# Kernel tuning notes

Hardware: AMD Instinct MI355X
Metric: run time of the kernel (lower is better)

The kernel has to match this reference:

```python
import jax, jax.numpy as jnp
import numpy as np

B, S, HID = 2, 2048, 2048
NH, NKV, HD = 16, 2, 128
N_REP = NH // NKV
SCALE = HD ** -0.5
NEG = -1e9


def rotate_half(x):
    x1, x2 = x[..., : HD // 2], x[..., HD // 2 :]
    return jnp.concatenate((-x2, x1), axis=-1)


def setup_inputs() -> dict:
    key = jax.random.key(0)
    ks = jax.random.split(key, 8)
    hidden_states = jax.random.normal(ks[0], (B, S, HID), jnp.float32)
    # RoPE tables (theta=10000), shape [B, S, HD]
    inv_freq = 1.0 / (10000.0 ** (np.arange(0, HD, 2, dtype=np.float32) / HD))
    pos = np.arange(S, dtype=np.float32)
    freqs = np.outer(pos, inv_freq)  # [S, HD/2]
    emb = np.concatenate([freqs, freqs], axis=-1)  # [S, HD]
    cos = jnp.broadcast_to(jnp.asarray(np.cos(emb)), (B, S, HD))
    sin = jnp.broadcast_to(jnp.asarray(np.sin(emb)), (B, S, HD))
    # additive causal mask [B, 1, S, S]
    causal = jnp.where(jnp.tril(jnp.ones((S, S), bool)), 0.0, NEG).astype(jnp.float32)
    attention_mask = jnp.broadcast_to(causal[None, None], (B, 1, S, S))
    sc = 0.02
    return {
        "hidden_states": hidden_states,
        "cos": cos,
        "sin": sin,
        "attention_mask": attention_mask,
        "Wq": jax.random.normal(ks[1], (NH * HD, HID), jnp.float32) * sc,
        "bq": jax.random.normal(ks[2], (NH * HD,), jnp.float32) * sc,
        "Wk": jax.random.normal(ks[3], (NKV * HD, HID), jnp.float32) * sc,
        "bk": jax.random.normal(ks[4], (NKV * HD,), jnp.float32) * sc,
        "Wv": jax.random.normal(ks[5], (NKV * HD, HID), jnp.float32) * sc,
        "bv": jax.random.normal(ks[6], (NKV * HD,), jnp.float32) * sc,
        "Wo": jax.random.normal(ks[7], (HID, NH * HD), jnp.float32) * sc,
    }


def reference(hidden_states, cos, sin, attention_mask, Wq, bq, Wk, bk, Wv, bv, Wo):
    b, s, _ = hidden_states.shape
    # QKV projections -> [B, H, S, D]
    q = (hidden_states @ Wq.T + bq).reshape(b, s, NH, HD).transpose(0, 2, 1, 3)
    k = (hidden_states @ Wk.T + bk).reshape(b, s, NKV, HD).transpose(0, 2, 1, 3)
    v = (hidden_states @ Wv.T + bv).reshape(b, s, NKV, HD).transpose(0, 2, 1, 3)
    # RoPE (cos/sin unsqueezed at head dim)
    c, si = cos[:, None], sin[:, None]
    q = q * c + rotate_half(q) * si
    k = k * c + rotate_half(k) * si
    # GQA: repeat kv heads
    k = jnp.repeat(k, N_REP, axis=1)
    v = jnp.repeat(v, N_REP, axis=1)
    scores = jnp.einsum("bhqd,bhkd->bhqk", q, k) * SCALE
    scores = scores + attention_mask[:, :, :, :s]
    attn_weights = jax.nn.softmax(scores.astype(jnp.float32), axis=-1).astype(q.dtype)
    attn_out = jnp.einsum("bhqk,bhkd->bhqd", attn_weights, v)
    attn_out = attn_out.transpose(0, 2, 1, 3).reshape(b, s, NH * HD)
    out = attn_out @ Wo.T
    return out, attn_weights
```

## Files before the change

kernel.cpp:

```cpp
#include <hip/hip_runtime.h>
#include <hip/hip_bf16.h>
#include <cstdint>

constexpr int Bb  = 2;
constexpr int Ss  = 2048;
constexpr int HID = 2048;
constexpr int NH  = 16;
constexpr int NKV = 2;
constexpr int HD  = 128;
constexpr int Mrows = Bb * Ss;
constexpr float SCALE = 0.08838834764831845f;

typedef __bf16 bf16_t;
typedef __attribute__((ext_vector_type(8))) __bf16 bf16x8;
typedef __attribute__((ext_vector_type(4))) __bf16 bf16x4;
typedef __attribute__((ext_vector_type(4))) float f32x4;

static __device__ __forceinline__ f32x4 mfma16(bf16x8 a, bf16x8 b, f32x4 c) {
  return __builtin_amdgcn_mfma_f32_16x16x32_bf16(a, b, c, 0, 0, 0);
}

static __device__ __forceinline__ void stage_async(bf16_t* lds, const bf16_t* src,
                                                   int ld, int tid) {
#pragma unroll
  for (int it = 0; it < 2; ++it) {
    int c = tid + it * 256;
    int row = c >> 2, kc = c & 3;
    __builtin_amdgcn_global_load_lds(
        (const __attribute__((address_space(1))) void*)(src + (size_t)row * ld + kc * 8),
        (__attribute__((address_space(3))) void*)(lds + c * 8), 16, 0, 0);
  }
}

template <int IM, int JM>
static __device__ __forceinline__ void wave_mma(const bf16_t* As, const bf16_t* Bs,
                                                f32x4 (&acc)[IM][JM], int wm, int wn,
                                                int lane) {
  const int q = lane >> 4, r = lane & 15;
  bf16x8 a[IM], b[JM];
#pragma unroll
  for (int i = 0; i < IM; ++i)
    a[i] = *(const bf16x8*)(As + (wm + i * 16 + r) * 32 + q * 8);
#pragma unroll
  for (int j = 0; j < JM; ++j)
    b[j] = *(const bf16x8*)(Bs + (wn + j * 16 + r) * 32 + q * 8);
#pragma unroll
  for (int i = 0; i < IM; ++i)
#pragma unroll
    for (int j = 0; j < JM; ++j)
      acc[i][j] = mfma16(a[i], b[j], acc[i][j]);
}

__global__ void cvt_bf16_kernel(const float* __restrict__ in, bf16_t* __restrict__ out) {
  size_t i = ((size_t)blockIdx.x * 256 + threadIdx.x) * 8;
  float4 a = *(const float4*)(in + i);
  float4 b = *(const float4*)(in + i + 4);
  bf16x8 v;
  v[0] = (__bf16)a.x; v[1] = (__bf16)a.y; v[2] = (__bf16)a.z; v[3] = (__bf16)a.w;
  v[4] = (__bf16)b.x; v[5] = (__bf16)b.y; v[6] = (__bf16)b.z; v[7] = (__bf16)b.w;
  *(bf16x8*)(out + i) = v;
}

__global__ void zero_kernel(float* __restrict__ p) {
  p[(size_t)blockIdx.x * 256 + threadIdx.x] = 0.0f;
}

__global__ __launch_bounds__(256) void proj_kernel(
    const bf16_t* __restrict__ A, const bf16_t* __restrict__ Bt,
    const float* __restrict__ bq, const float* __restrict__ bk,
    const float* __restrict__ bv, const float* __restrict__ cosb,
    const float* __restrict__ sinb, bf16_t* __restrict__ q_bf,
    bf16_t* __restrict__ k_bf, bf16_t* __restrict__ v_t) {
  __shared__ __align__(16) bf16_t As[128 * 32];
  __shared__ __align__(16) bf16_t Bs[128 * 32];
  const int tid = threadIdx.x;
  const int bx = blockIdx.x;
  const int m0 = blockIdx.y * 128, n0 = bx * 128;
  const int lane = tid & 63, w = tid >> 6;
  const int wm = w * 32;
  const int q = lane >> 4, r = lane & 15;
  f32x4 acc[2][8];
#pragma unroll
  for (int i = 0; i < 2; ++i)
#pragma unroll
    for (int j = 0; j < 8; ++j) acc[i][j] = (f32x4){0.f, 0.f, 0.f, 0.f};
  const bf16_t* Ap = A + (size_t)m0 * HID;
  const bf16_t* Bp = Bt + (size_t)n0 * HID;
  for (int k0 = 0; k0 < HID; k0 += 32) {
    stage_async(As, Ap + k0, HID, tid);
    stage_async(Bs, Bp + k0, HID, tid);
    __syncthreads();
    wave_mma<2, 8>(As, Bs, acc, wm, 0, lane);
    __syncthreads();
  }
  const float* bias_base;
  int mode;
  int hh;
  if (bx < 16) { mode = 0; hh = bx; bias_base = bq + n0; }
  else if (bx < 18) { mode = 1; hh = bx - 16; bias_base = bk + (bx - 16) * 128; }
  else { mode = 2; hh = bx - 18; bias_base = bv + (bx - 18) * 128; }
  float bias_j[8];
#pragma unroll
  for (int j = 0; j < 8; ++j) bias_j[j] = bias_base[j * 16 + r];
  float e[2][8][4];
#pragma unroll
  for (int i = 0; i < 2; ++i)
#pragma unroll
    for (int j = 0; j < 8; ++j)
#pragma unroll
      for (int t = 0; t < 4; ++t) e[i][j][t] = acc[i][j][t] + bias_j[j];

  if (mode == 2) {
#pragma unroll
    for (int i = 0; i < 2; ++i) {
      int s_base = m0 + wm + i * 16 + q * 4;
      int bI = s_base >> 11, s = s_base & 2047;
#pragma unroll
      for (int j = 0; j < 8; ++j) {
        int d = j * 16 + r;
        bf16x4 pk;
#pragma unroll
        for (int t = 0; t < 4; ++t) pk[t] = (__bf16)e[i][j][t];
        *(bf16x4*)(v_t + ((size_t)(bI * NKV + hh) * HD + d) * Ss + s) = pk;
      }
    }
  } else {
    bf16_t* dst_base = (mode == 0) ? q_bf : k_bf;
    const int nhv = (mode == 0) ? NH : NKV;
#pragma unroll
    for (int i = 0; i < 2; ++i) {
#pragma unroll
      for (int t = 0; t < 4; ++t) {
        int s_glob = m0 + wm + i * 16 + q * 4 + t;
        int bI = s_glob >> 11, s = s_glob & 2047;
        const float* cp = cosb + ((size_t)bI * Ss + s) * HD;
        const float* sp = sinb + ((size_t)bI * Ss + s) * HD;
        bf16_t* dst = dst_base + ((size_t)(bI * nhv + hh) * Ss + s) * HD;
#pragma unroll
        for (int j = 0; j < 8; ++j) {
          int d = j * 16 + r;
          float c = cp[d], sn = sp[d];
          float p = e[i][j ^ 4][t];
          float o = e[i][j][t] * c + ((j < 4) ? -p : p) * sn;
          dst[d] = (__bf16)o;
        }
      }
    }
  }
}

__global__ __launch_bounds__(256) void qk_kernel(const bf16_t* __restrict__ qb,
                                                 const bf16_t* __restrict__ kb,
                                                 float* __restrict__ attn,
                                                 float* __restrict__ rowsum) {
  const int tj = blockIdx.x, ti = blockIdx.y;
  if (tj > ti) return;
  const int bh = blockIdx.z;
  const int b = bh >> 4, h = bh & 15, kv = h >> 3;
  __shared__ __align__(16) bf16_t As[128 * 32];
  __shared__ __align__(16) bf16_t Bs[128 * 32];
  __shared__ float rs[128];
  const int tid = threadIdx.x;
  if (tid < 128) rs[tid] = 0.0f;
  const int lane = tid & 63, w = tid >> 6;
  const int wm = (w >> 1) * 64, wn = (w & 1) * 64;
  const int q = lane >> 4, r = lane & 15;
  f32x4 acc[4][4];
#pragma unroll
  for (int i = 0; i < 4; ++i)
#pragma unroll
    for (int j = 0; j < 4; ++j) acc[i][j] = (f32x4){0.f, 0.f, 0.f, 0.f};
  const bf16_t* Ap = qb + (size_t)bh * Ss * HD + (size_t)ti * 128 * HD;
  const bf16_t* Bp = kb + (size_t)(b * NKV + kv) * Ss * HD + (size_t)tj * 128 * HD;
#pragma unroll
  for (int k0 = 0; k0 < HD; k0 += 32) {
    stage_async(As, Ap + k0, HD, tid);
    stage_async(Bs, Bp + k0, HD, tid);
    __syncthreads();
    wave_mma<4, 4>(As, Bs, acc, wm, wn, lane);
    __syncthreads();
  }
  const bool diag = (ti == tj);
  float rp[4][4];
#pragma unroll
  for (int i = 0; i < 4; ++i)
#pragma unroll
    for (int t = 0; t < 4; ++t) rp[i][t] = 0.0f;
  float* orow = attn + ((size_t)bh * Ss + (size_t)ti * 128) * Ss + (size_t)tj * 128;
#pragma unroll
  for (int i = 0; i < 4; ++i) {
#pragma unroll
    for (int t = 0; t < 4; ++t) {
      int row_l = wm + i * 16 + q * 4 + t;
#pragma unroll
      for (int j = 0; j < 4; ++j) {
        int col_l = wn + j * 16 + r;
        float ev = (diag && col_l > row_l) ? 0.0f : __expf(acc[i][j][t] * SCALE);
        orow[(size_t)row_l * Ss + col_l] = ev;
        rp[i][t] += ev;
      }
    }
  }
#pragma unroll
  for (int off = 1; off < 16; off <<= 1)
#pragma unroll
    for (int i = 0; i < 4; ++i)
#pragma unroll
      for (int t = 0; t < 4; ++t) rp[i][t] += __shfl_xor(rp[i][t], off, 64);
  if (r == 0) {
#pragma unroll
    for (int i = 0; i < 4; ++i)
#pragma unroll
      for (int t = 0; t < 4; ++t)
        atomicAdd(&rs[wm + i * 16 + q * 4 + t], rp[i][t]);
  }
  __syncthreads();
  if (tid < 128)
    atomicAdd(rowsum + (size_t)bh * Ss + (size_t)ti * 128 + tid, rs[tid]);
}

__global__ __launch_bounds__(256) void pv_kernel(float* __restrict__ attn,
                                                 const bf16_t* __restrict__ vt,
                                                 const float* __restrict__ rowsum,
                                                 bf16_t* __restrict__ ao) {
  const int mt = blockIdx.y;
  const int bh = blockIdx.z;
  const int b = bh >> 4, h = bh & 15, kv = h >> 3;
  __shared__ __align__(16) bf16_t As[128 * 32];
  __shared__ __align__(16) bf16_t Bs[128 * 32];
  __shared__ float inv_s[128];
  const int tid = threadIdx.x;
  if (tid < 128)
    inv_s[tid] = 1.0f / rowsum[(size_t)bh * Ss + (size_t)mt * 128 + tid];
  __syncthreads();
  const int lane = tid & 63, w = tid >> 6;
  const int wm = (w >> 1) * 64, wn = (w & 1) * 64;
  const int q = lane >> 4, r = lane & 15;
  f32x4 acc[4][4];
#pragma unroll
  for (int i = 0; i < 4; ++i)
#pragma unroll
    for (int j = 0; j < 4; ++j) acc[i][j] = (f32x4){0.f, 0.f, 0.f, 0.f};
  float* Ap = attn + (size_t)bh * Ss * Ss + (size_t)mt * 128 * Ss;
  const bf16_t* Bp = vt + (size_t)(b * NKV + kv) * HD * Ss;
  const int kmax = (mt + 1) * 128;
  for (int k0 = 0; k0 < kmax; k0 += 32) {
#pragma unroll
    for (int it = 0; it < 2; ++it) {
      int c = tid + it * 256;
      int row = c >> 2, kc = c & 3;
      float* p = Ap + (size_t)row * Ss + k0 + kc * 8;
      float4 a = *(const float4*)p;
      float4 bq4 = *(const float4*)(p + 4);
      float inv = inv_s[row];
      a.x *= inv; a.y *= inv; a.z *= inv; a.w *= inv;
      bq4.x *= inv; bq4.y *= inv; bq4.z *= inv; bq4.w *= inv;
      *(float4*)p = a;
      *(float4*)(p + 4) = bq4;
      bf16x8 v8;
      v8[0] = (__bf16)a.x; v8[1] = (__bf16)a.y; v8[2] = (__bf16)a.z; v8[3] = (__bf16)a.w;
      v8[4] = (__bf16)bq4.x; v8[5] = (__bf16)bq4.y; v8[6] = (__bf16)bq4.z; v8[7] = (__bf16)bq4.w;
      *(bf16x8*)(As + c * 8) = v8;
    }
    stage_async(Bs, Bp + k0, Ss, tid);
    __syncthreads();
    wave_mma<4, 4>(As, Bs, acc, wm, wn, lane);
    __syncthreads();
  }
  const int width = Ss - kmax;
  if (width > 0) {
    const float4 z4 = {0.f, 0.f, 0.f, 0.f};
    for (int rr = 0; rr < 128; ++rr) {
      float* zp = Ap + (size_t)rr * Ss + kmax;
      for (int cc = tid * 4; cc < width; cc += 1024) *(float4*)(zp + cc) = z4;
    }
  }
#pragma unroll
  for (int i = 0; i < 4; ++i) {
#pragma unroll
    for (int t = 0; t < 4; ++t) {
      int row = mt * 128 + wm + i * 16 + q * 4 + t;
#pragma unroll
      for (int j = 0; j < 4; ++j) {
        int col = wn + j * 16 + r;
        ao[(((size_t)b * Ss + row) * NH + h) * HD + col] = (__bf16)acc[i][j][t];
      }
    }
  }
}

__global__ __launch_bounds__(256) void out_kernel(const bf16_t* __restrict__ A,
                                                  const bf16_t* __restrict__ Bt,
                                                  float* __restrict__ outp) {
  __shared__ __align__(16) bf16_t As[128 * 32];
  __shared__ __align__(16) bf16_t Bs[128 * 32];
  const int tid = threadIdx.x;
  const int m0 = blockIdx.y * 128, n0 = blockIdx.x * 128;
  const int lane = tid & 63, w = tid >> 6;
  const int wm = (w >> 1) * 64, wn = (w & 1) * 64;
  const int q = lane >> 4, r = lane & 15;
  f32x4 acc[4][4];
#pragma unroll
  for (int i = 0; i < 4; ++i)
#pragma unroll
    for (int j = 0; j < 4; ++j) acc[i][j] = (f32x4){0.f, 0.f, 0.f, 0.f};
  const bf16_t* Ap = A + (size_t)m0 * HID;
  const bf16_t* Bp = Bt + (size_t)n0 * HID;
  for (int k0 = 0; k0 < HID; k0 += 32) {
    stage_async(As, Ap + k0, HID, tid);
    stage_async(Bs, Bp + k0, HID, tid);
    __syncthreads();
    wave_mma<4, 4>(As, Bs, acc, wm, wn, lane);
    __syncthreads();
  }
#pragma unroll
  for (int i = 0; i < 4; ++i) {
#pragma unroll
    for (int t = 0; t < 4; ++t) {
      int row = m0 + wm + i * 16 + q * 4 + t;
#pragma unroll
      for (int j = 0; j < 4; ++j) {
        int col = n0 + wn + j * 16 + r;
        outp[(size_t)row * HID + col] = acc[i][j][t];
      }
    }
  }
}

extern "C" void kernel_launch(void* const* d_in, const int* in_sizes, int n_in,
                              void* d_out, int out_size, void* d_ws, size_t ws_size,
                              hipStream_t stream) {
  const float* hs   = (const float*)d_in[0];
  const float* cosb = (const float*)d_in[1];
  const float* sinb = (const float*)d_in[2];
  const float* Wq = (const float*)d_in[4];
  const float* bq = (const float*)d_in[5];
  const float* Wk = (const float*)d_in[6];
  const float* bk = (const float*)d_in[7];
  const float* Wv = (const float*)d_in[8];
  const float* bv = (const float*)d_in[9];
  const float* Wo = (const float*)d_in[10];

  float* out  = (float*)d_out;
  float* attn = out + (size_t)Bb * Ss * HID;

  char* wsp = (char*)d_ws;
  auto alloc = [&](size_t bytes) -> char* {
    char* p = wsp;
    wsp += (bytes + 255) & ~(size_t)255;
    return p;
  };
  bf16_t* hs_bf = (bf16_t*)alloc((size_t)Mrows * HID * 2);
  bf16_t* wqkv  = (bf16_t*)alloc((size_t)2560 * HID * 2);
  bf16_t* wo_bf = (bf16_t*)alloc((size_t)HID * NH * HD * 2);
  bf16_t* q_bf  = (bf16_t*)alloc((size_t)Mrows * NH * HD * 2);
  bf16_t* k_bf  = (bf16_t*)alloc((size_t)Bb * NKV * Ss * HD * 2);
  bf16_t* v_t   = (bf16_t*)alloc((size_t)Bb * NKV * Ss * HD * 2);
  bf16_t* ao_bf = (bf16_t*)alloc((size_t)Mrows * NH * HD * 2);
  float*  rs_ws = (float*)alloc((size_t)Bb * NH * Ss * 4);

  zero_kernel<<<(Bb * NH * Ss) / 256, 256, 0, stream>>>(rs_ws);

  cvt_bf16_kernel<<<(Mrows * HID) / 2048, 256, 0, stream>>>(hs, hs_bf);
  cvt_bf16_kernel<<<(NH * HD * HID) / 2048, 256, 0, stream>>>(Wq, wqkv);
  cvt_bf16_kernel<<<(NKV * HD * HID) / 2048, 256, 0, stream>>>(Wk, wqkv + (size_t)2048 * HID);
  cvt_bf16_kernel<<<(NKV * HD * HID) / 2048, 256, 0, stream>>>(Wv, wqkv + (size_t)2304 * HID);
  cvt_bf16_kernel<<<(HID * NH * HD) / 2048, 256, 0, stream>>>(Wo, wo_bf);

  proj_kernel<<<dim3(20, 32), 256, 0, stream>>>(hs_bf, wqkv, bq, bk, bv, cosb, sinb,
                                                q_bf, k_bf, v_t);

  qk_kernel<<<dim3(16, 16, Bb * NH), 256, 0, stream>>>(q_bf, k_bf, attn, rs_ws);

  pv_kernel<<<dim3(1, 16, Bb * NH), 256, 0, stream>>>(attn, v_t, rs_ws, ao_bf);

  out_kernel<<<dim3(16, 32), 256, 0, stream>>>(ao_bf, wo_bf, out);

  (void)in_sizes; (void)n_in; (void)out_size; (void)ws_size;
}
```

Baseline: 1.079 ms.

## Recompute QK scores in PV kernel instead of round-tripping fp32 attn matrix

The first pass now computes only the exp row sums and no longer writes the unnormalised scores. A new fused kernel recomputes QK^T per key tile, normalises with the precomputed row sums, writes the final attention weights once, and feeds them through LDS in bf16 straight into the PV matmul. This removes one full write plus a read and rewrite of the large fp32 attention matrix, at the cost of doing the QK matmul twice. The fused kernel also uses more LDS and registers, and its launch grid has only one block per query tile per head.

```diff
diff --git a/kernel.cpp b/kernel.cpp
--- a/kernel.cpp
+++ b/kernel.cpp
@@ -149,9 +149,8 @@
   }
 }
 
-__global__ __launch_bounds__(256) void qk_kernel(const bf16_t* __restrict__ qb,
+__global__ __launch_bounds__(256) void qs_kernel(const bf16_t* __restrict__ qb,
                                                  const bf16_t* __restrict__ kb,
-                                                 float* __restrict__ attn,
                                                  float* __restrict__ rowsum) {
   const int tj = blockIdx.x, ti = blockIdx.y;
   if (tj > ti) return;
@@ -186,7 +185,6 @@
   for (int i = 0; i < 4; ++i)
 #pragma unroll
     for (int t = 0; t < 4; ++t) rp[i][t] = 0.0f;
-  float* orow = attn + ((size_t)bh * Ss + (size_t)ti * 128) * Ss + (size_t)tj * 128;
 #pragma unroll
   for (int i = 0; i < 4; ++i) {
 #pragma unroll
@@ -196,7 +194,6 @@
       for (int j = 0; j < 4; ++j) {
         int col_l = wn + j * 16 + r;
         float ev = (diag && col_l > row_l) ? 0.0f : __expf(acc[i][j][t] * SCALE);
-        orow[(size_t)row_l * Ss + col_l] = ev;
         rp[i][t] += ev;
       }
     }
@@ -219,59 +216,121 @@
     atomicAdd(rowsum + (size_t)bh * Ss + (size_t)ti * 128 + tid, rs[tid]);
 }
 
-__global__ __launch_bounds__(256) void pv_kernel(float* __restrict__ attn,
-                                                 const bf16_t* __restrict__ vt,
-                                                 const float* __restrict__ rowsum,
-                                                 bf16_t* __restrict__ ao) {
+__global__ __launch_bounds__(256, 2) void spv_kernel(
+    const bf16_t* __restrict__ qb, const bf16_t* __restrict__ kb,
+    const bf16_t* __restrict__ vt, const float* __restrict__ rowsum,
+    float* __restrict__ attn, bf16_t* __restrict__ ao) {
   const int mt = blockIdx.y;
   const int bh = blockIdx.z;
   const int b = bh >> 4, h = bh & 15, kv = h >> 3;
-  __shared__ __align__(16) bf16_t As[128 * 32];
-  __shared__ __align__(16) bf16_t Bs[128 * 32];
+  __shared__ __align__(16) bf16_t Ks[4][128 * 32];
+  __shared__ __align__(16) bf16_t Ps[128 * 136];
   __shared__ float inv_s[128];
   const int tid = threadIdx.x;
   if (tid < 128)
     inv_s[tid] = 1.0f / rowsum[(size_t)bh * Ss + (size_t)mt * 128 + tid];
-  __syncthreads();
   const int lane = tid & 63, w = tid >> 6;
   const int wm = (w >> 1) * 64, wn = (w & 1) * 64;
   const int q = lane >> 4, r = lane & 15;
-  f32x4 acc[4][4];
+
+  const bf16_t* Qp = qb + (size_t)bh * Ss * HD + (size_t)mt * 128 * HD;
+#pragma unroll
+  for (int s = 0; s < 4; ++s) stage_async(Ks[s], Qp + s * 32, HD, tid);
+  __syncthreads();
+  bf16x8 aq[4][4];
+#pragma unroll
+  for (int s = 0; s < 4; ++s)
+#pragma unroll
+    for (int i = 0; i < 4; ++i)
+      aq[s][i] = *(const bf16x8*)(Ks[s] + (wm + i * 16 + r) * 32 + q * 8);
+  float inv_my[4][4];
 #pragma unroll
   for (int i = 0; i < 4; ++i)
 #pragma unroll
-    for (int j = 0; j < 4; ++j) acc[i][j] = (f32x4){0.f, 0.f, 0.f, 0.f};
-  float* Ap = attn + (size_t)bh * Ss * Ss + (size_t)mt * 128 * Ss;
-  const bf16_t* Bp = vt + (size_t)(b * NKV + kv) * HD * Ss;
+    for (int t = 0; t < 4; ++t)
+      inv_my[i][t] = inv_s[wm + i * 16 + q * 4 + t];
+  __syncthreads();
+
+  const bf16_t* Kp = kb + (size_t)(b * NKV + kv) * Ss * HD;
+  const bf16_t* Vp = vt + (size_t)(b * NKV + kv) * HD * Ss;
+  float* Arow = attn + ((size_t)bh * Ss + (size_t)mt * 128) * Ss;
+
+  f32x4 acc2[4][4];
+#pragma unroll
+  for (int i = 0; i < 4; ++i)
+#pragma unroll
+    for (int j = 0; j < 4; ++j) acc2[i][j] = (f32x4){0.f, 0.f, 0.f, 0.f};
+
+  for (int kt = 0; kt <= mt; ++kt) {
+#pragma unroll
+    for (int s = 0; s < 4; ++s)
+      stage_async(Ks[s], Kp + (size_t)kt * 128 * HD + s * 32, HD, tid);
+    __syncthreads();
+    f32x4 acc[4][4];
+#pragma unroll
+    for (int i = 0; i < 4; ++i)
+#pragma unroll
+      for (int j = 0; j < 4; ++j) acc[i][j] = (f32x4){0.f, 0.f, 0.f, 0.f};
+#pragma unroll
+    for (int s = 0; s < 4; ++s) {
+      bf16x8 bfr[4];
+#pragma unroll
+      for (int j = 0; j < 4; ++j)
+        bfr[j] = *(const bf16x8*)(Ks[s] + (wn + j * 16 + r) * 32 + q * 8);
+#pragma unroll
+      for (int i = 0; i < 4; ++i)
+#pragma unroll
+        for (int j = 0; j < 4; ++j)
+          acc[i][j] = mfma16(aq[s][i], bfr[j], acc[i][j]);
+    }
+    const bool diag = (kt == mt);
+#pragma unroll
+    for (int i = 0; i < 4; ++i) {
+#pragma unroll
+      for (int t = 0; t < 4; ++t) {
+        int row_l = wm + i * 16 + q * 4 + t;
+        float inv = inv_my[i][t];
+        float* orow = Arow + (size_t)row_l * Ss + kt * 128;
+#pragma unroll
+        for (int j = 0; j < 4; ++j) {
+          int col_l = wn + j * 16 + r;
+          float ev = (diag && col_l > row_l)
+                         ? 0.0f
+                         : __expf(acc[i][j][t] * SCALE) * inv;
+          orow[col_l] = ev;
+          Ps[row_l * 136 + col_l] = (__bf16)ev;
+        }
+      }
+    }
+    __syncthreads();
+#pragma unroll
+    for (int s = 0; s < 4; ++s)
+      stage_async(Ks[s], Vp + kt * 128 + s * 32, Ss, tid);
+    __syncthreads();
+#pragma unroll
+    for (int s = 0; s < 4; ++s) {
+      bf16x8 ap[4], bv4[4];
+#pragma unroll
+      for (int i = 0; i < 4; ++i)
+        ap[i] = *(const bf16x8*)(Ps + (wm + i * 16 + r) * 136 + s * 32 + q * 8);
+#pragma unroll
+      for (int j = 0; j < 4; ++j)
+        bv4[j] = *(const bf16x8*)(Ks[s] + (wn + j * 16 + r) * 32 + q * 8);
+#pragma unroll
+      for (int i = 0; i < 4; ++i)
+#pragma unroll
+        for (int j = 0; j < 4; ++j)
+          acc2[i][j] = mfma16(ap[i], bv4[j], acc2[i][j]);
+    }
+    __syncthreads();
+  }
+
   const int kmax = (mt + 1) * 128;
-  for (int k0 = 0; k0 < kmax; k0 += 32) {
-#pragma unroll
-    for (int it = 0; it < 2; ++it) {
-      int c = tid + it * 256;
-      int row = c >> 2, kc = c & 3;
-      float* p = Ap + (size_t)row * Ss + k0 + kc * 8;
-      float4 a = *(const float4*)p;
-      float4 bq4 = *(const float4*)(p + 4);
-      float inv = inv_s[row];
-      a.x *= inv; a.y *= inv; a.z *= inv; a.w *= inv;
-      bq4.x *= inv; bq4.y *= inv; bq4.z *= inv; bq4.w *= inv;
-      *(float4*)p = a;
-      *(float4*)(p + 4) = bq4;
-      bf16x8 v8;
-      v8[0] = (__bf16)a.x; v8[1] = (__bf16)a.y; v8[2] = (__bf16)a.z; v8[3] = (__bf16)a.w;
-      v8[4] = (__bf16)bq4.x; v8[5] = (__bf16)bq4.y; v8[6] = (__bf16)bq4.z; v8[7] = (__bf16)bq4.w;
-      *(bf16x8*)(As + c * 8) = v8;
-    }
-    stage_async(Bs, Bp + k0, Ss, tid);
-    __syncthreads();
-    wave_mma<4, 4>(As, Bs, acc, wm, wn, lane);
-    __syncthreads();
-  }
   const int width = Ss - kmax;
   if (width > 0) {
     const float4 z4 = {0.f, 0.f, 0.f, 0.f};
     for (int rr = 0; rr < 128; ++rr) {
-      float* zp = Ap + (size_t)rr * Ss + kmax;
+      float* zp = Arow + (size_t)rr * Ss + kmax;
       for (int cc = tid * 4; cc < width; cc += 1024) *(float4*)(zp + cc) = z4;
     }
   }
@@ -283,7 +342,7 @@
 #pragma unroll
       for (int j = 0; j < 4; ++j) {
         int col = wn + j * 16 + r;
-        ao[(((size_t)b * Ss + row) * NH + h) * HD + col] = (__bf16)acc[i][j][t];
+        ao[(((size_t)b * Ss + row) * NH + h) * HD + col] = (__bf16)acc2[i][j][t];
       }
     }
   }
@@ -370,9 +429,10 @@
   proj_kernel<<<dim3(20, 32), 256, 0, stream>>>(hs_bf, wqkv, bq, bk, bv, cosb, sinb,
                                                 q_bf, k_bf, v_t);
 
-  qk_kernel<<<dim3(16, 16, Bb * NH), 256, 0, stream>>>(q_bf, k_bf, attn, rs_ws);
-
-  pv_kernel<<<dim3(1, 16, Bb * NH), 256, 0, stream>>>(attn, v_t, rs_ws, ao_bf);
+  qs_kernel<<<dim3(16, 16, Bb * NH), 256, 0, stream>>>(q_bf, k_bf, rs_ws);
+
+  spv_kernel<<<dim3(1, 16, Bb * NH), 256, 0, stream>>>(q_bf, k_bf, v_t, rs_ws,
+                                                       attn, ao_bf);
 
   out_kernel<<<dim3(16, 32), 256, 0, stream>>>(ao_bf, wo_bf, out);
 
```

Result: faster. 1.004 ms (-7.0%).
